# Performance work log

Measured on AMD Instinct MI355X. Metric: run time of the kernel, lower is better.

## Reference

```python
import jax, jax.numpy as jnp
import numpy as np
import math

N, E = 50000, 1600000
IN, HID, OUT, ED, H = 128, 32, 64, 64, 4
HC = H * HID  # 128, input dim of second layer


def setup_inputs() -> dict:
    key = jax.random.key(0)
    ks = jax.random.split(key, 32)
    w = lambda k, shape: (jax.random.normal(k, shape, jnp.float32) * 0.05)
    inp = {
        "x": w(ks[0], (N, IN)),
        "edge_feats": w(ks[1], (E, ED)),
        "edge_index": jax.random.randint(ks[2], (2, E), 0, N, jnp.int32),
        # layer 1: TransformerConv(IN -> HID, heads=H, concat=True, edge_dim=ED)
        "Wq1": w(ks[3], (IN, HC)), "bq1": w(ks[4], (HC,)),
        "Wk1": w(ks[5], (IN, HC)), "bk1": w(ks[6], (HC,)),
        "Wv1": w(ks[7], (IN, HC)), "bv1": w(ks[8], (HC,)),
        "We1": w(ks[9], (ED, HC)),  # lin_edge has no bias in PyG
        "Ws1": w(ks[10], (IN, HC)), "bs1": w(ks[11], (HC,)),
        # layer 2: TransformerConv(HC -> OUT, heads=1, concat=False, edge_dim=ED)
        "Wq2": w(ks[12], (HC, OUT)), "bq2": w(ks[13], (OUT,)),
        "Wk2": w(ks[14], (HC, OUT)), "bk2": w(ks[15], (OUT,)),
        "Wv2": w(ks[16], (HC, OUT)), "bv2": w(ks[17], (OUT,)),
        "We2": w(ks[18], (ED, OUT)),
        "Ws2": w(ks[19], (HC, OUT)), "bs2": w(ks[20], (OUT,)),
    }
    return inp


def tconv(x, src, dst, ef, Wq, bq, Wk, bk, Wv, bv, We, Ws, bs, heads, ch, concat):
    """PyG TransformerConv (beta=False, root_weight=True), eval mode."""
    n = x.shape[0]
    q = (x @ Wq + bq).reshape(n, heads, ch)
    k = (x @ Wk + bk).reshape(n, heads, ch)
    v = (x @ Wv + bv).reshape(n, heads, ch)
    e = (ef @ We).reshape(-1, heads, ch)           # [E,H,C]
    k_j = k[src] + e                                # gather + edge bias
    v_j = v[src] + e
    alpha = jnp.einsum("ehc,ehc->eh", q[dst], k_j) / math.sqrt(ch)  # [E,H]
    # segment softmax over destination nodes
    m = jax.lax.stop_gradient(jax.ops.segment_max(alpha, dst, num_segments=n))
    a = jnp.exp(alpha - m[dst])
    den = jax.ops.segment_sum(a, dst, num_segments=n)
    a = a / den[dst]
    msg = v_j * a[..., None]                        # [E,H,C]
    out = jax.ops.segment_sum(msg, dst, num_segments=n)  # [N,H,C]
    out = out.reshape(n, heads * ch) if concat else out.mean(axis=1)
    return out + x @ Ws + bs                        # root/skip connection


def reference(x, edge_feats, edge_index, Wq1, bq1, Wk1, bk1, Wv1, bv1, We1, Ws1, bs1,
              Wq2, bq2, Wk2, bk2, Wv2, bv2, We2, Ws2, bs2):
    src, dst = edge_index[0], edge_index[1]
    h = tconv(x, src, dst, edge_feats, Wq1, bq1, Wk1, bk1, Wv1, bv1, We1, Ws1, bs1,
              H, HID, True)
    h = jax.nn.relu(h)  # dropout=0.0 (eval) -> identity
    out = tconv(h, src, dst, edge_feats, Wq2, bq2, Wk2, bk2, Wv2, bv2, We2, Ws2, bs2,
                1, OUT, False)
    return out
```

## Files before the change

### kernel.cpp

```cpp
#include <hip/hip_runtime.h>

#define NN 50000
#define EE 1600000

__device__ inline float b2f(unsigned short u) {
    return __uint_as_float(((unsigned)u) << 16);
}
__device__ inline unsigned short f2bf(float f) {
    unsigned u = __float_as_uint(f);
    unsigned r = 0x7fffu + ((u >> 16) & 1u);
    return (unsigned short)((u + r) >> 16);
}
__device__ inline void stv(float* p, size_t i, float v) { p[i] = v; }
__device__ inline void stv(unsigned short* p, size_t i, float v) { p[i] = f2bf(v); }

__global__ void sniff_kernel(const void* w, int* flags) {
    int lane = threadIdx.x;
    const unsigned short* u = (const unsigned short*)w;
    int bad = 0;
    for (int i = lane; i < 256; i += 64) {
        float f = b2f(u[i]);
        if (!(fabsf(f) < 2.0f)) bad++;
    }
    unsigned long long m = __ballot(bad > 0);
    if (lane == 0) {
        flags[0] = (__popcll(m) > 8) ? 1 : 0;
        flags[1] = 0;
    }
}

struct WTab {
    const void* p[18];
    int off[18];
    int sz[18];
};
__global__ void __launch_bounds__(256) convert_kernel(WTab t, const int* __restrict__ flags,
                                                      unsigned short* __restrict__ dst) {
    int f32 = flags[0];
    int ti = blockIdx.y;
    int i = blockIdx.x * 256 + threadIdx.x;
    if (i < t.sz[ti]) {
        dst[t.off[ti] + i] = f32 ? f2bf(((const float*)t.p[ti])[i])
                                 : ((const unsigned short*)t.p[ti])[i];
    }
}

__global__ void __launch_bounds__(256) count_kernel(const int* __restrict__ dst,
                                                    int* __restrict__ cnt) {
    int e = blockIdx.x * 256 + threadIdx.x;
    if (e < EE) atomicAdd(&cnt[dst[e]], 1);
}

__global__ void __launch_bounds__(1024) scan_kernel(int* __restrict__ cntfill,
                                                    int* __restrict__ rowptr) {
    __shared__ int s[1024];
    __shared__ int carry_s;
    int tid = threadIdx.x;
    if (tid == 0) carry_s = 0;
    __syncthreads();
    for (int base = 0; base < NN; base += 4096) {
        int i0 = base + tid * 4;
        int v0 = (i0 + 0 < NN) ? cntfill[i0 + 0] : 0;
        int v1 = (i0 + 1 < NN) ? cntfill[i0 + 1] : 0;
        int v2 = (i0 + 2 < NN) ? cntfill[i0 + 2] : 0;
        int v3 = (i0 + 3 < NN) ? cntfill[i0 + 3] : 0;
        int tsum = v0 + v1 + v2 + v3;
        s[tid] = tsum;
        __syncthreads();
        for (int off = 1; off < 1024; off <<= 1) {
            int t = (tid >= off) ? s[tid - off] : 0;
            __syncthreads();
            s[tid] += t;
            __syncthreads();
        }
        int carry = carry_s;
        int excl = carry + s[tid] - tsum;
        int e0 = excl, e1 = excl + v0, e2 = e1 + v1, e3 = e2 + v2;
        if (i0 + 0 < NN) { rowptr[i0 + 0] = e0; cntfill[i0 + 0] = e0; }
        if (i0 + 1 < NN) { rowptr[i0 + 1] = e1; cntfill[i0 + 1] = e1; }
        if (i0 + 2 < NN) { rowptr[i0 + 2] = e2; cntfill[i0 + 2] = e2; }
        if (i0 + 3 < NN) { rowptr[i0 + 3] = e3; cntfill[i0 + 3] = e3; }
        __syncthreads();
        if (tid == 1023) carry_s = carry + s[1023];
        __syncthreads();
    }
    if (tid == 0) rowptr[NN] = carry_s;
}

__global__ void __launch_bounds__(256) fill_kernel(const int* __restrict__ dst,
                                                   int* __restrict__ cntfill,
                                                   int* __restrict__ perm) {
    int e = blockIdx.x * 256 + threadIdx.x;
    if (e < EE) {
        int p = atomicAdd(&cntfill[dst[e]], 1);
        perm[p] = e;
    }
}

template <typename TO, int K, int OD, int TR>
__global__ void __launch_bounds__(256) gemm_node(const void* __restrict__ X,
                                                 const int* __restrict__ flagp,
                                                 const unsigned short* __restrict__ W,
                                                 const unsigned short* __restrict__ bias,
                                                 TO* __restrict__ C, int nrows) {
    constexpr int TRP = TR + 4;
    __shared__ unsigned short Ws[K * OD];
    __shared__ float Xs[K * TRP];
    int tid = threadIdx.x;
    int xf32 = *flagp;
    for (int i = tid; i < K * OD; i += 256) Ws[i] = W[i];
    int row0 = blockIdx.x * TR;
    const float* Xf = (const float*)X;
    const unsigned short* Xu = (const unsigned short*)X;
    for (int i = tid; i < TR * K; i += 256) {
        int r = i / K, kk = i % K;
        int rr = row0 + r;
        float vv = 0.f;
        if (rr < nrows) {
            size_t idx = (size_t)rr * K + kk;
            vv = xf32 ? Xf[idx] : b2f(Xu[idx]);
        }
        Xs[kk * TRP + r] = vv;
    }
    __syncthreads();
    constexpr int CG = OD / 4;
    int rg = tid / CG, cg = tid % CG;
    int r0 = rg * 4, c0 = cg * 4;
    float acc[4][4] = {};
#pragma unroll 4
    for (int kk = 0; kk < K; ++kk) {
        const float4 xv = *(const float4*)&Xs[kk * TRP + r0];
        ushort4 wu = *(const ushort4*)&Ws[kk * OD + c0];
        float xa[4] = {xv.x, xv.y, xv.z, xv.w};
        float wb[4] = {b2f(wu.x), b2f(wu.y), b2f(wu.z), b2f(wu.w)};
#pragma unroll
        for (int i2 = 0; i2 < 4; i2++)
#pragma unroll
            for (int j2 = 0; j2 < 4; j2++) acc[i2][j2] += xa[i2] * wb[j2];
    }
    float bb[4];
#pragma unroll
    for (int j2 = 0; j2 < 4; j2++) bb[j2] = b2f(bias[c0 + j2]);
#pragma unroll
    for (int i2 = 0; i2 < 4; i2++) {
        int rr = row0 + r0 + i2;
        if (rr < nrows) {
#pragma unroll
            for (int j2 = 0; j2 < 4; j2++)
                stv(C, (size_t)rr * OD + c0 + j2, acc[i2][j2] + bb[j2]);
        }
    }
}

__global__ void __launch_bounds__(256) qe1_kernel(const unsigned short* __restrict__ q,
                                                  const unsigned short* __restrict__ We,
                                                  float* __restrict__ qe) {
    __shared__ float Ws[64 * 129];
    __shared__ float qs[8 * 128];
    int tid = threadIdx.x;
    for (int i = tid; i < 64 * 128; i += 256) Ws[(i / 128) * 129 + (i % 128)] = b2f(We[i]);
    int n0 = blockIdx.x * 8;
    for (int i = tid; i < 8 * 128; i += 256) {
        int n = n0 + (i >> 7);
        qs[i] = (n < NN) ? b2f(q[(size_t)n * 128 + (i & 127)]) : 0.f;
    }
    __syncthreads();
    int h = tid >> 6, d = tid & 63;
    for (int nl = 0; nl < 8; ++nl) {
        int n = n0 + nl;
        if (n < NN) {
            float acc = 0.f;
#pragma unroll
            for (int c = 0; c < 32; ++c)
                acc += qs[nl * 128 + h * 32 + c] * Ws[d * 129 + h * 32 + c];
            qe[(size_t)n * 256 + h * 64 + d] = acc;
        }
    }
}

__global__ void __launch_bounds__(256) qe2_kernel(const unsigned short* __restrict__ q,
                                                  const unsigned short* __restrict__ We,
                                                  float* __restrict__ qe) {
    __shared__ float Ws[64 * 65];
    __shared__ float qs[4 * 64];
    int tid = threadIdx.x;
    for (int i = tid; i < 64 * 64; i += 256) Ws[(i / 64) * 65 + (i % 64)] = b2f(We[i]);
    int n0 = blockIdx.x * 4;
    {
        int n = n0 + (tid >> 6);
        qs[tid] = (n < NN) ? b2f(q[(size_t)n * 64 + (tid & 63)]) : 0.f;
    }
    __syncthreads();
    int nl = tid >> 6, d = tid & 63;
    int n = n0 + nl;
    if (n < NN) {
        float acc = 0.f;
#pragma unroll
        for (int c = 0; c < 64; ++c) acc += qs[nl * 64 + c] * Ws[d * 65 + c];
        qe[(size_t)n * 64 + d] = acc;
    }
}

__global__ void __launch_bounds__(256) node_pass1(
    const int* __restrict__ rowptr, const int* __restrict__ perm,
    const int* __restrict__ src, const unsigned short* __restrict__ q,
    const unsigned short* __restrict__ k, const unsigned short* __restrict__ v,
    const float* __restrict__ qe, const void* __restrict__ efp,
    const int* __restrict__ flagp, float* __restrict__ av, float* __restrict__ wef) {
    int lane = threadIdx.x & 63;
    int node = (blockIdx.x * 256 + threadIdx.x) >> 6;
    if (node >= NN) return;
    int ef32 = *flagp;
    const float* efF = (const float*)efp;
    const unsigned short* efU = (const unsigned short*)efp;
    int h = lane & 3;
    int dq = lane >> 2;
    int c1 = h * 32 + dq, c2 = c1 + 16;
    float qa = b2f(q[(size_t)node * 128 + c1]);
    float qb = b2f(q[(size_t)node * 128 + c2]);
    const float* qer = qe + (size_t)node * 256 + h * 64 + dq;
    float qm0 = qer[0], qm1 = qer[16], qm2 = qer[32], qm3 = qer[48];
    float m = -__builtin_inff(), l = 0.f, a1 = 0.f, a2 = 0.f;
    float w0 = 0.f, w1 = 0.f, w2 = 0.f, w3 = 0.f;
    int beg = rowptr[node], end = rowptr[node + 1];
    const float rs = 0.17677669529663687f;
    for (int i = beg; i < end; ++i) {
        int e = perm[i];
        int sj = src[e];
        const unsigned short* kr = k + (size_t)sj * 128;
        const unsigned short* vr = v + (size_t)sj * 128;
        float f0, f1, f2, f3;
        if (ef32) {
            const float* er = efF + (size_t)e * 64;
            f0 = er[dq]; f1 = er[dq + 16]; f2 = er[dq + 32]; f3 = er[dq + 48];
        } else {
            const unsigned short* er = efU + (size_t)e * 64;
            f0 = b2f(er[dq]); f1 = b2f(er[dq + 16]);
            f2 = b2f(er[dq + 32]); f3 = b2f(er[dq + 48]);
        }
        float kv1 = b2f(kr[c1]), kv2 = b2f(kr[c2]);
        float vv1 = b2f(vr[c1]), vv2 = b2f(vr[c2]);
        float t = qa * kv1 + qb * kv2 + qm0 * f0 + qm1 * f1 + qm2 * f2 + qm3 * f3;
        t += __shfl_xor(t, 4);
        t += __shfl_xor(t, 8);
        t += __shfl_xor(t, 16);
        t += __shfl_xor(t, 32);
        float alpha = t * rs;
        float mn = fmaxf(m, alpha);
        float sc = __expf(m - mn);
        float w = __expf(alpha - mn);
        m = mn;
        l = l * sc + w;
        a1 = a1 * sc + w * vv1;
        a2 = a2 * sc + w * vv2;
        w0 = w0 * sc + w * f0;
        w1 = w1 * sc + w * f1;
        w2 = w2 * sc + w * f2;
        w3 = w3 * sc + w * f3;
    }
    float inv = (l > 0.f) ? 1.f / l : 0.f;
    av[(size_t)node * 128 + c1] = a1 * inv;
    av[(size_t)node * 128 + c2] = a2 * inv;
    float* wr = wef + (size_t)node * 256 + h * 64 + dq;
    wr[0] = w0 * inv;
    wr[16] = w1 * inv;
    wr[32] = w2 * inv;
    wr[48] = w3 * inv;
}

__global__ void __launch_bounds__(256) node_pass2(
    const int* __restrict__ rowptr, const int* __restrict__ perm,
    const int* __restrict__ src, const unsigned short* __restrict__ q,
    const unsigned short* __restrict__ k, const unsigned short* __restrict__ v,
    const float* __restrict__ qe, const void* __restrict__ efp,
    const int* __restrict__ flagp, float* __restrict__ av, float* __restrict__ wef) {
    int lane = threadIdx.x & 63;
    int node = (blockIdx.x * 256 + threadIdx.x) >> 6;
    if (node >= NN) return;
    int ef32 = *flagp;
    const float* efF = (const float*)efp;
    const unsigned short* efU = (const unsigned short*)efp;
    float qa = b2f(q[(size_t)node * 64 + lane]);
    float qj = qe[(size_t)node * 64 + lane];
    float m = -__builtin_inff(), l = 0.f, a1 = 0.f, w0 = 0.f;
    int beg = rowptr[node], end = rowptr[node + 1];
    for (int i = beg; i < end; ++i) {
        int e = perm[i];
        int sj = src[e];
        float fj = ef32 ? efF[(size_t)e * 64 + lane] : b2f(efU[(size_t)e * 64 + lane]);
        float kv = b2f(k[(size_t)sj * 64 + lane]);
        float vv = b2f(v[(size_t)sj * 64 + lane]);
        float t = qa * kv + qj * fj;
        t += __shfl_xor(t, 1);
        t += __shfl_xor(t, 2);
        t += __shfl_xor(t, 4);
        t += __shfl_xor(t, 8);
        t += __shfl_xor(t, 16);
        t += __shfl_xor(t, 32);
        float alpha = t * 0.125f;
        float mn = fmaxf(m, alpha);
        float sc = __expf(m - mn);
        float w = __expf(alpha - mn);
        m = mn;
        l = l * sc + w;
        a1 = a1 * sc + w * vv;
        w0 = w0 * sc + w * fj;
    }
    float inv = (l > 0.f) ? 1.f / l : 0.f;
    av[(size_t)node * 64 + lane] = a1 * inv;
    wef[(size_t)node * 64 + lane] = w0 * inv;
}

__global__ void __launch_bounds__(256) ep1_kernel(const float* __restrict__ av,
                                                  const float* __restrict__ wef,
                                                  const float* __restrict__ s1,
                                                  const unsigned short* __restrict__ We,
                                                  unsigned short* __restrict__ hout) {
    __shared__ float Ws[64 * 128];
    int tid = threadIdx.x;
    for (int i = tid; i < 64 * 128; i += 256) Ws[i] = b2f(We[i]);
    __syncthreads();
    int nl = tid >> 7;
    int c = tid & 127;
    int g = c >> 5;
    for (int it = 0; it < 8; ++it) {
        int n = blockIdx.x * 16 + it * 2 + nl;
        if (n < NN) {
            const float* wr = wef + (size_t)n * 256 + g * 64;
            float acc = 0.f;
#pragma unroll
            for (int d = 0; d < 64; ++d) acc += wr[d] * Ws[d * 128 + c];
            float val = av[(size_t)n * 128 + c] + acc + s1[(size_t)n * 128 + c];
            hout[(size_t)n * 128 + c] = f2bf(fmaxf(val, 0.f));
        }
    }
}

__global__ void __launch_bounds__(256) ep2_kernel(const float* __restrict__ av,
                                                  const float* __restrict__ wef,
                                                  const float* __restrict__ s2,
                                                  const unsigned short* __restrict__ We,
                                                  float* __restrict__ out) {
    __shared__ float Ws[64 * 64];
    int tid = threadIdx.x;
    for (int i = tid; i < 64 * 64; i += 256) Ws[i] = b2f(We[i]);
    __syncthreads();
    int nl = tid >> 6;
    int c = tid & 63;
    for (int it = 0; it < 4; ++it) {
        int n = blockIdx.x * 16 + it * 4 + nl;
        if (n < NN) {
            const float* wr = wef + (size_t)n * 64;
            float acc = 0.f;
#pragma unroll
            for (int d = 0; d < 64; ++d) acc += wr[d] * Ws[d * 64 + c];
            float val = av[(size_t)n * 64 + c] + acc + s2[(size_t)n * 64 + c];
            out[(size_t)n * 64 + c] = val;
        }
    }
}

extern "C" void kernel_launch(void* const* d_in, const int* in_sizes, int n_in,
                              void* d_out, int out_size, void* d_ws, size_t ws_size,
                              hipStream_t stream) {
    (void)in_sizes; (void)n_in; (void)out_size; (void)ws_size;
    const int* eidx = (const int*)d_in[2];
    const int* src = eidx;
    const int* dst = eidx + EE;

    char* p = (char*)d_ws;
    auto alloc = [&](size_t bytes) {
        void* r = (void*)p;
        p += (bytes + 255) & ~(size_t)255;
        return r;
    };
    unsigned short* wts = (unsigned short*)alloc(111360 * 2);
    int* flags          = (int*)alloc(256);
    int* rowptr         = (int*)alloc((size_t)(NN + 1) * 4);
    int* cntfill        = (int*)alloc((size_t)(NN + 1) * 4);
    int* perm           = (int*)alloc((size_t)EE * 4);
    unsigned short* q1  = (unsigned short*)alloc((size_t)NN * 128 * 2);
    unsigned short* k1  = (unsigned short*)alloc((size_t)NN * 128 * 2);
    unsigned short* v1  = (unsigned short*)alloc((size_t)NN * 128 * 2);
    float* qe           = (float*)alloc((size_t)NN * 256 * 4);
    float* av           = (float*)alloc((size_t)NN * 128 * 4);
    float* wef          = (float*)alloc((size_t)NN * 256 * 4);

    WTab tab;
    int off = 0;
    const int wsz[18] = {16384, 128, 16384, 128, 16384, 128, 8192, 16384, 128,
                         8192, 64, 8192, 64, 8192, 64, 4096, 8192, 64};
    int offs[18];
    for (int i = 0; i < 18; ++i) {
        tab.p[i] = d_in[3 + i];
        tab.sz[i] = wsz[i];
        tab.off[i] = off;
        offs[i] = off;
        off += wsz[i];
    }
    const unsigned short* Wq1c = wts + offs[0];
    const unsigned short* bq1c = wts + offs[1];
    const unsigned short* Wk1c = wts + offs[2];
    const unsigned short* bk1c = wts + offs[3];
    const unsigned short* Wv1c = wts + offs[4];
    const unsigned short* bv1c = wts + offs[5];
    const unsigned short* We1c = wts + offs[6];
    const unsigned short* Ws1c = wts + offs[7];
    const unsigned short* bs1c = wts + offs[8];
    const unsigned short* Wq2c = wts + offs[9];
    const unsigned short* bq2c = wts + offs[10];
    const unsigned short* Wk2c = wts + offs[11];
    const unsigned short* bk2c = wts + offs[12];
    const unsigned short* Wv2c = wts + offs[13];
    const unsigned short* bv2c = wts + offs[14];
    const unsigned short* We2c = wts + offs[15];
    const unsigned short* Ws2c = wts + offs[16];
    const unsigned short* bs2c = wts + offs[17];

    hipMemsetAsync(cntfill, 0, (size_t)(NN + 1) * 4, stream);
    sniff_kernel<<<1, 64, 0, stream>>>(d_in[3], flags);
    convert_kernel<<<dim3(64, 18), 256, 0, stream>>>(tab, flags, wts);
    count_kernel<<<EE / 256, 256, 0, stream>>>(dst, cntfill);
    scan_kernel<<<1, 1024, 0, stream>>>(cntfill, rowptr);
    fill_kernel<<<EE / 256, 256, 0, stream>>>(dst, cntfill, perm);

    int g1 = (NN + 31) / 32;
    gemm_node<unsigned short, 128, 128, 32><<<g1, 256, 0, stream>>>(d_in[0], flags, Wq1c, bq1c, q1, NN);
    gemm_node<unsigned short, 128, 128, 32><<<g1, 256, 0, stream>>>(d_in[0], flags, Wk1c, bk1c, k1, NN);
    gemm_node<unsigned short, 128, 128, 32><<<g1, 256, 0, stream>>>(d_in[0], flags, Wv1c, bv1c, v1, NN);
    qe1_kernel<<<(NN + 7) / 8, 256, 0, stream>>>(q1, We1c, qe);
    node_pass1<<<(NN + 3) / 4, 256, 0, stream>>>(rowptr, perm, src, q1, k1, v1, qe,
                                                 d_in[1], flags, av, wef);
    float* s1 = qe;
    gemm_node<float, 128, 128, 32><<<g1, 256, 0, stream>>>(d_in[0], flags, Ws1c, bs1c, s1, NN);
    unsigned short* h = k1;
    ep1_kernel<<<(NN + 15) / 16, 256, 0, stream>>>(av, wef, s1, We1c, h);

    unsigned short* q2 = q1;
    unsigned short* k2 = q1 + (size_t)NN * 64;
    unsigned short* v2 = v1;
    float* s2 = qe;
    float* qe2 = av;
    float* av2 = av + (size_t)NN * 64;
    float* wef2 = wef;
    int g2 = (NN + 63) / 64;
    gemm_node<unsigned short, 128, 64, 64><<<g2, 256, 0, stream>>>(h, flags + 1, Wq2c, bq2c, q2, NN);
    gemm_node<unsigned short, 128, 64, 64><<<g2, 256, 0, stream>>>(h, flags + 1, Wk2c, bk2c, k2, NN);
    gemm_node<unsigned short, 128, 64, 64><<<g2, 256, 0, stream>>>(h, flags + 1, Wv2c, bv2c, v2, NN);
    gemm_node<float, 128, 64, 64><<<g2, 256, 0, stream>>>(h, flags + 1, Ws2c, bs2c, s2, NN);
    qe2_kernel<<<(NN + 3) / 4, 256, 0, stream>>>(q2, We2c, qe2);
    node_pass2<<<(NN + 3) / 4, 256, 0, stream>>>(rowptr, perm, src, q2, k2, v2, qe2,
                                                 d_in[1], flags, av2, wef2);
    ep2_kernel<<<(NN + 15) / 16, 256, 0, stream>>>(av2, wef2, s2, We2c,
                                                   (float*)d_out);
}
```

Measured before the change: 1.981 ms.

## Interleave K/V rows and batch four edges per softmax step in gather passes

```diff
diff --git a/kernel.cpp b/kernel.cpp
--- a/kernel.cpp
+++ b/kernel.cpp
@@ -102,7 +102,8 @@
                                                  const int* __restrict__ flagp,
                                                  const unsigned short* __restrict__ W,
                                                  const unsigned short* __restrict__ bias,
-                                                 TO* __restrict__ C, int nrows) {
+                                                 TO* __restrict__ C, int nrows,
+                                                 int ldc, int cstride, int coff) {
     constexpr int TRP = TR + 4;
     __shared__ unsigned short Ws[K * OD];
     __shared__ float Xs[K * TRP];
@@ -147,7 +148,8 @@
         if (rr < nrows) {
 #pragma unroll
             for (int j2 = 0; j2 < 4; j2++)
-                stv(C, (size_t)rr * OD + c0 + j2, acc[i2][j2] + bb[j2]);
+                stv(C, (size_t)rr * ldc + (size_t)(c0 + j2) * cstride + coff,
+                    acc[i2][j2] + bb[j2]);
         }
     }
 }
@@ -204,7 +206,7 @@
 __global__ void __launch_bounds__(256) node_pass1(
     const int* __restrict__ rowptr, const int* __restrict__ perm,
     const int* __restrict__ src, const unsigned short* __restrict__ q,
-    const unsigned short* __restrict__ k, const unsigned short* __restrict__ v,
+    const unsigned short* __restrict__ kv,
     const float* __restrict__ qe, const void* __restrict__ efp,
     const int* __restrict__ flagp, float* __restrict__ av, float* __restrict__ wef) {
     int lane = threadIdx.x & 63;
@@ -218,60 +220,128 @@
     int c1 = h * 32 + dq, c2 = c1 + 16;
     float qa = b2f(q[(size_t)node * 128 + c1]);
     float qb = b2f(q[(size_t)node * 128 + c2]);
-    const float* qer = qe + (size_t)node * 256 + h * 64 + dq;
-    float qm0 = qer[0], qm1 = qer[16], qm2 = qer[32], qm3 = qer[48];
+    float4 qm = *(const float4*)(qe + (size_t)node * 256 + h * 64 + 4 * dq);
     float m = -__builtin_inff(), l = 0.f, a1 = 0.f, a2 = 0.f;
     float w0 = 0.f, w1 = 0.f, w2 = 0.f, w3 = 0.f;
     int beg = rowptr[node], end = rowptr[node + 1];
     const float rs = 0.17677669529663687f;
-    for (int i = beg; i < end; ++i) {
+
+    int nn4 = (end - beg) & ~3;
+    int lim = beg + nn4;
+    int i = beg;
+    int ee[4], ss[4];
+    if (nn4 > 0) {
+#pragma unroll
+        for (int u = 0; u < 4; ++u) ee[u] = perm[i + u];
+#pragma unroll
+        for (int u = 0; u < 4; ++u) ss[u] = src[ee[u]];
+    }
+    for (; i < lim; i += 4) {
+        unsigned kua[4], kub[4];
+        float f0[4], f1[4], f2[4], f3[4];
+#pragma unroll
+        for (int u = 0; u < 4; ++u) {
+            const unsigned short* kr = kv + (size_t)ss[u] * 256;
+            kua[u] = *(const unsigned*)(kr + 2 * c1);
+            kub[u] = *(const unsigned*)(kr + 2 * c2);
+        }
+        if (ef32) {
+#pragma unroll
+            for (int u = 0; u < 4; ++u) {
+                float4 fv = *(const float4*)(efF + (size_t)ee[u] * 64 + 4 * dq);
+                f0[u] = fv.x; f1[u] = fv.y; f2[u] = fv.z; f3[u] = fv.w;
+            }
+        } else {
+#pragma unroll
+            for (int u = 0; u < 4; ++u) {
+                ushort4 fu = *(const ushort4*)(efU + (size_t)ee[u] * 64 + 4 * dq);
+                f0[u] = b2f(fu.x); f1[u] = b2f(fu.y); f2[u] = b2f(fu.z); f3[u] = b2f(fu.w);
+            }
+        }
+        if (i + 8 <= lim) {
+#pragma unroll
+            for (int u = 0; u < 4; ++u) ee[u] = perm[i + 4 + u];
+#pragma unroll
+            for (int u = 0; u < 4; ++u) ss[u] = src[ee[u]];
+        }
+        float t[4];
+#pragma unroll
+        for (int u = 0; u < 4; ++u) {
+            float ka = b2f((unsigned short)(kua[u] & 0xffffu));
+            float kb = b2f((unsigned short)(kub[u] & 0xffffu));
+            float tt = qa * ka + qb * kb + qm.x * f0[u] + qm.y * f1[u] +
+                       qm.z * f2[u] + qm.w * f3[u];
+            tt += __shfl_xor(tt, 4);
+            tt += __shfl_xor(tt, 8);
+            tt += __shfl_xor(tt, 16);
+            tt += __shfl_xor(tt, 32);
+            t[u] = tt * rs;
+        }
+        float mn = fmaxf(fmaxf(fmaxf(t[0], t[1]), fmaxf(t[2], t[3])), m);
+        float sc = __expf(m - mn);
+        float w[4];
+#pragma unroll
+        for (int u = 0; u < 4; ++u) w[u] = __expf(t[u] - mn);
+        m = mn;
+        l = l * sc + ((w[0] + w[1]) + (w[2] + w[3]));
+        float sa1 = 0.f, sa2 = 0.f, sw0 = 0.f, sw1 = 0.f, sw2 = 0.f, sw3 = 0.f;
+#pragma unroll
+        for (int u = 0; u < 4; ++u) {
+            float va = b2f((unsigned short)(kua[u] >> 16));
+            float vb = b2f((unsigned short)(kub[u] >> 16));
+            sa1 += w[u] * va; sa2 += w[u] * vb;
+            sw0 += w[u] * f0[u]; sw1 += w[u] * f1[u];
+            sw2 += w[u] * f2[u]; sw3 += w[u] * f3[u];
+        }
+        a1 = a1 * sc + sa1; a2 = a2 * sc + sa2;
+        w0 = w0 * sc + sw0; w1 = w1 * sc + sw1;
+        w2 = w2 * sc + sw2; w3 = w3 * sc + sw3;
+    }
+    for (; i < end; ++i) {
         int e = perm[i];
         int sj = src[e];
-        const unsigned short* kr = k + (size_t)sj * 128;
-        const unsigned short* vr = v + (size_t)sj * 128;
-        float f0, f1, f2, f3;
+        const unsigned short* kr = kv + (size_t)sj * 256;
+        unsigned kua = *(const unsigned*)(kr + 2 * c1);
+        unsigned kub = *(const unsigned*)(kr + 2 * c2);
+        float f0s, f1s, f2s, f3s;
         if (ef32) {
-            const float* er = efF + (size_t)e * 64;
-            f0 = er[dq]; f1 = er[dq + 16]; f2 = er[dq + 32]; f3 = er[dq + 48];
+            float4 fv = *(const float4*)(efF + (size_t)e * 64 + 4 * dq);
+            f0s = fv.x; f1s = fv.y; f2s = fv.z; f3s = fv.w;
         } else {
-            const unsigned short* er = efU + (size_t)e * 64;
-            f0 = b2f(er[dq]); f1 = b2f(er[dq + 16]);
-            f2 = b2f(er[dq + 32]); f3 = b2f(er[dq + 48]);
-        }
-        float kv1 = b2f(kr[c1]), kv2 = b2f(kr[c2]);
-        float vv1 = b2f(vr[c1]), vv2 = b2f(vr[c2]);
-        float t = qa * kv1 + qb * kv2 + qm0 * f0 + qm1 * f1 + qm2 * f2 + qm3 * f3;
-        t += __shfl_xor(t, 4);
-        t += __shfl_xor(t, 8);
-        t += __shfl_xor(t, 16);
-        t += __shfl_xor(t, 32);
-        float alpha = t * rs;
+            ushort4 fu = *(const ushort4*)(efU + (size_t)e * 64 + 4 * dq);
+            f0s = b2f(fu.x); f1s = b2f(fu.y); f2s = b2f(fu.z); f3s = b2f(fu.w);
+        }
+        float ka = b2f((unsigned short)(kua & 0xffffu));
+        float kb = b2f((unsigned short)(kub & 0xffffu));
+        float tt = qa * ka + qb * kb + qm.x * f0s + qm.y * f1s + qm.z * f2s + qm.w * f3s;
+        tt += __shfl_xor(tt, 4);
+        tt += __shfl_xor(tt, 8);
+        tt += __shfl_xor(tt, 16);
+        tt += __shfl_xor(tt, 32);
+        float alpha = tt * rs;
         float mn = fmaxf(m, alpha);
         float sc = __expf(m - mn);
         float w = __expf(alpha - mn);
         m = mn;
         l = l * sc + w;
-        a1 = a1 * sc + w * vv1;
-        a2 = a2 * sc + w * vv2;
-        w0 = w0 * sc + w * f0;
-        w1 = w1 * sc + w * f1;
-        w2 = w2 * sc + w * f2;
-        w3 = w3 * sc + w * f3;
+        float va = b2f((unsigned short)(kua >> 16));
+        float vb = b2f((unsigned short)(kub >> 16));
+        a1 = a1 * sc + w * va;
+        a2 = a2 * sc + w * vb;
+        w0 = w0 * sc + w * f0s; w1 = w1 * sc + w * f1s;
+        w2 = w2 * sc + w * f2s; w3 = w3 * sc + w * f3s;
     }
     float inv = (l > 0.f) ? 1.f / l : 0.f;
     av[(size_t)node * 128 + c1] = a1 * inv;
     av[(size_t)node * 128 + c2] = a2 * inv;
-    float* wr = wef + (size_t)node * 256 + h * 64 + dq;
-    wr[0] = w0 * inv;
-    wr[16] = w1 * inv;
-    wr[32] = w2 * inv;
-    wr[48] = w3 * inv;
+    float4 wout = make_float4(w0 * inv, w1 * inv, w2 * inv, w3 * inv);
+    *(float4*)(wef + (size_t)node * 256 + h * 64 + 4 * dq) = wout;
 }
 
 __global__ void __launch_bounds__(256) node_pass2(
     const int* __restrict__ rowptr, const int* __restrict__ perm,
     const int* __restrict__ src, const unsigned short* __restrict__ q,
-    const unsigned short* __restrict__ k, const unsigned short* __restrict__ v,
+    const unsigned short* __restrict__ kv,
     const float* __restrict__ qe, const void* __restrict__ efp,
     const int* __restrict__ flagp, float* __restrict__ av, float* __restrict__ wef) {
     int lane = threadIdx.x & 63;
@@ -284,25 +354,86 @@
     float qj = qe[(size_t)node * 64 + lane];
     float m = -__builtin_inff(), l = 0.f, a1 = 0.f, w0 = 0.f;
     int beg = rowptr[node], end = rowptr[node + 1];
-    for (int i = beg; i < end; ++i) {
+
+    int nn4 = (end - beg) & ~3;
+    int lim = beg + nn4;
+    int i = beg;
+    int ee[4], ss[4];
+    if (nn4 > 0) {
+#pragma unroll
+        for (int u = 0; u < 4; ++u) ee[u] = perm[i + u];
+#pragma unroll
+        for (int u = 0; u < 4; ++u) ss[u] = src[ee[u]];
+    }
+    for (; i < lim; i += 4) {
+        unsigned ku[4];
+        float fj[4];
+#pragma unroll
+        for (int u = 0; u < 4; ++u)
+            ku[u] = *(const unsigned*)(kv + (size_t)ss[u] * 128 + 2 * lane);
+        if (ef32) {
+#pragma unroll
+            for (int u = 0; u < 4; ++u) fj[u] = efF[(size_t)ee[u] * 64 + lane];
+        } else {
+#pragma unroll
+            for (int u = 0; u < 4; ++u) fj[u] = b2f(efU[(size_t)ee[u] * 64 + lane]);
+        }
+        if (i + 8 <= lim) {
+#pragma unroll
+            for (int u = 0; u < 4; ++u) ee[u] = perm[i + 4 + u];
+#pragma unroll
+            for (int u = 0; u < 4; ++u) ss[u] = src[ee[u]];
+        }
+        float t[4];
+#pragma unroll
+        for (int u = 0; u < 4; ++u) {
+            float kk = b2f((unsigned short)(ku[u] & 0xffffu));
+            float tt = qa * kk + qj * fj[u];
+            tt += __shfl_xor(tt, 1);
+            tt += __shfl_xor(tt, 2);
+            tt += __shfl_xor(tt, 4);
+            tt += __shfl_xor(tt, 8);
+            tt += __shfl_xor(tt, 16);
+            tt += __shfl_xor(tt, 32);
+            t[u] = tt * 0.125f;
+        }
+        float mn = fmaxf(fmaxf(fmaxf(t[0], t[1]), fmaxf(t[2], t[3])), m);
+        float sc = __expf(m - mn);
+        float w[4];
+#pragma unroll
+        for (int u = 0; u < 4; ++u) w[u] = __expf(t[u] - mn);
+        m = mn;
+        l = l * sc + ((w[0] + w[1]) + (w[2] + w[3]));
+        float sa = 0.f, sw = 0.f;
+#pragma unroll
+        for (int u = 0; u < 4; ++u) {
+            float vv = b2f((unsigned short)(ku[u] >> 16));
+            sa += w[u] * vv;
+            sw += w[u] * fj[u];
+        }
+        a1 = a1 * sc + sa;
+        w0 = w0 * sc + sw;
+    }
+    for (; i < end; ++i) {
         int e = perm[i];
         int sj = src[e];
+        unsigned ku = *(const unsigned*)(kv + (size_t)sj * 128 + 2 * lane);
         float fj = ef32 ? efF[(size_t)e * 64 + lane] : b2f(efU[(size_t)e * 64 + lane]);
-        float kv = b2f(k[(size_t)sj * 64 + lane]);
-        float vv = b2f(v[(size_t)sj * 64 + lane]);
-        float t = qa * kv + qj * fj;
-        t += __shfl_xor(t, 1);
-        t += __shfl_xor(t, 2);
-        t += __shfl_xor(t, 4);
-        t += __shfl_xor(t, 8);
-        t += __shfl_xor(t, 16);
-        t += __shfl_xor(t, 32);
-        float alpha = t * 0.125f;
+        float kk = b2f((unsigned short)(ku & 0xffffu));
+        float tt = qa * kk + qj * fj;
+        tt += __shfl_xor(tt, 1);
+        tt += __shfl_xor(tt, 2);
+        tt += __shfl_xor(tt, 4);
+        tt += __shfl_xor(tt, 8);
+        tt += __shfl_xor(tt, 16);
+        tt += __shfl_xor(tt, 32);
+        float alpha = tt * 0.125f;
         float mn = fmaxf(m, alpha);
         float sc = __expf(m - mn);
         float w = __expf(alpha - mn);
         m = mn;
         l = l * sc + w;
+        float vv = b2f((unsigned short)(ku >> 16));
         a1 = a1 * sc + w * vv;
         w0 = w0 * sc + w * fj;
     }
@@ -380,8 +511,7 @@
     int* cntfill        = (int*)alloc((size_t)(NN + 1) * 4);
     int* perm           = (int*)alloc((size_t)EE * 4);
     unsigned short* q1  = (unsigned short*)alloc((size_t)NN * 128 * 2);
-    unsigned short* k1  = (unsigned short*)alloc((size_t)NN * 128 * 2);
-    unsigned short* v1  = (unsigned short*)alloc((size_t)NN * 128 * 2);
+    unsigned short* kv1 = (unsigned short*)alloc((size_t)NN * 256 * 2);
     float* qe           = (float*)alloc((size_t)NN * 256 * 4);
     float* av           = (float*)alloc((size_t)NN * 128 * 4);
     float* wef          = (float*)alloc((size_t)NN * 256 * 4);
@@ -425,31 +555,30 @@
     fill_kernel<<<EE / 256, 256, 0, stream>>>(dst, cntfill, perm);
 
     int g1 = (NN + 31) / 32;
-    gemm_node<unsigned short, 128, 128, 32><<<g1, 256, 0, stream>>>(d_in[0], flags, Wq1c, bq1c, q1, NN);
-    gemm_node<unsigned short, 128, 128, 32><<<g1, 256, 0, stream>>>(d_in[0], flags, Wk1c, bk1c, k1, NN);
-    gemm_node<unsigned short, 128, 128, 32><<<g1, 256, 0, stream>>>(d_in[0], flags, Wv1c, bv1c, v1, NN);
+    gemm_node<unsigned short, 128, 128, 32><<<g1, 256, 0, stream>>>(d_in[0], flags, Wq1c, bq1c, q1, NN, 128, 1, 0);
+    gemm_node<unsigned short, 128, 128, 32><<<g1, 256, 0, stream>>>(d_in[0], flags, Wk1c, bk1c, kv1, NN, 256, 2, 0);
+    gemm_node<unsigned short, 128, 128, 32><<<g1, 256, 0, stream>>>(d_in[0], flags, Wv1c, bv1c, kv1, NN, 256, 2, 1);
     qe1_kernel<<<(NN + 7) / 8, 256, 0, stream>>>(q1, We1c, qe);
-    node_pass1<<<(NN + 3) / 4, 256, 0, stream>>>(rowptr, perm, src, q1, k1, v1, qe,
+    node_pass1<<<(NN + 3) / 4, 256, 0, stream>>>(rowptr, perm, src, q1, kv1, qe,
                                                  d_in[1], flags, av, wef);
     float* s1 = qe;
-    gemm_node<float, 128, 128, 32><<<g1, 256, 0, stream>>>(d_in[0], flags, Ws1c, bs1c, s1, NN);
-    unsigned short* h = k1;
+    gemm_node<float, 128, 128, 32><<<g1, 256, 0, stream>>>(d_in[0], flags, Ws1c, bs1c, s1, NN, 128, 1, 0);
+    unsigned short* h = kv1;
     ep1_kernel<<<(NN + 15) / 16, 256, 0, stream>>>(av, wef, s1, We1c, h);
 
     unsigned short* q2 = q1;
-    unsigned short* k2 = q1 + (size_t)NN * 64;
-    unsigned short* v2 = v1;
+    unsigned short* kv2 = kv1 + (size_t)NN * 128;
     float* s2 = qe;
     float* qe2 = av;
     float* av2 = av + (size_t)NN * 64;
     float* wef2 = wef;
     int g2 = (NN + 63) / 64;
-    gemm_node<unsigned short, 128, 64, 64><<<g2, 256, 0, stream>>>(h, flags + 1, Wq2c, bq2c, q2, NN);
-    gemm_node<unsigned short, 128, 64, 64><<<g2, 256, 0, stream>>>(h, flags + 1, Wk2c, bk2c, k2, NN);
-    gemm_node<unsigned short, 128, 64, 64><<<g2, 256, 0, stream>>>(h, flags + 1, Wv2c, bv2c, v2, NN);
-    gemm_node<float, 128, 64, 64><<<g2, 256, 0, stream>>>(h, flags + 1, Ws2c, bs2c, s2, NN);
+    gemm_node<unsigned short, 128, 64, 64><<<g2, 256, 0, stream>>>(h, flags + 1, Wq2c, bq2c, q2, NN, 64, 1, 0);
+    gemm_node<unsigned short, 128, 64, 64><<<g2, 256, 0, stream>>>(h, flags + 1, Wk2c, bk2c, kv2, NN, 128, 2, 0);
+    gemm_node<unsigned short, 128, 64, 64><<<g2, 256, 0, stream>>>(h, flags + 1, Wv2c, bv2c, kv2, NN, 128, 2, 1);
+    gemm_node<float, 128, 64, 64><<<g2, 256, 0, stream>>>(h, flags + 1, Ws2c, bs2c, s2, NN, 64, 1, 0);
     qe2_kernel<<<(NN + 3) / 4, 256, 0, stream>>>(q2, We2c, qe2);
-    node_pass2<<<(NN + 3) / 4, 256, 0, stream>>>(rowptr, perm, src, q2, k2, v2, qe2,
+    node_pass2<<<(NN + 3) / 4, 256, 0, stream>>>(rowptr, perm, src, q2, kv2, qe2,
                                                  d_in[1], flags, av2, wef2);
     ep2_kernel<<<(NN + 15) / 16, 256, 0, stream>>>(av2, wef2, s2, We2c,
                                                    (float*)d_out);
```

New measurement: 1.676 ms. 1.18x faster.
